# Kernel optimization log

Hardware: AMD Instinct MI355X
Metric: run time of the kernel (lower is better)

The kernel has to match this reference:

```python
import jax, jax.numpy as jnp
import numpy as np

EPS = 1e-12  # torch F.normalize eps


def _l2norm(x, axis):
    n = jnp.maximum(jnp.linalg.norm(x, axis=axis, keepdims=True), EPS)
    return x / n


def setup_inputs() -> dict:
    key = jax.random.key(0)
    k1, k2, k3, k4, k5 = jax.random.split(key, 5)
    N, E, IN_DIM, FAC_K, DIM_K = 100000, 1600000, 64, 4, 16
    all_emb = jax.random.normal(k1, (N, IN_DIM), dtype=jnp.float32) * 0.1
    W = jax.random.normal(k2, (FAC_K, IN_DIM, DIM_K), dtype=jnp.float32) * (1.0 / np.sqrt(IN_DIM))
    b = jax.random.normal(k3, (FAC_K, 1, DIM_K), dtype=jnp.float32) * 0.02
    row = jax.random.randint(k4, (E,), 0, N, dtype=jnp.int32)
    col = jax.random.randint(k5, (E,), 0, N, dtype=jnp.int32)
    return {"all_emb": all_emb, "W": W, "b": b, "row": row, "col": col, "iter_k": 2}


def reference(all_emb, W, b, row, col, iter_k):
    N = all_emb.shape[0]
    # factorized projection: [N, in_dim] x [K, in_dim, dk] -> [K, N, dk]
    fac = jnp.einsum('nd,kdf->knf', all_emb, W + b)
    fac = jax.nn.leaky_relu(fac, negative_slope=0.2)
    fac = _l2norm(fac, axis=2)

    new_fac = fac
    for _ in range(iter_k):
        head = new_fac[:, row]            # [K, E, dk]
        tail = fac[:, col]                # [K, E, dk]
        p_uv = jnp.sum(head * tail, axis=2)   # [K, E]
        p_uv = jax.nn.softmax(p_uv, axis=0)   # softmax over factors
        p_uv = jax.lax.stop_gradient(p_uv)    # original detaches attention
        msg = p_uv[:, :, None] * tail         # [K, E, dk]
        agg = jax.vmap(lambda m: jax.ops.segment_sum(m, row, num_segments=N))(msg)
        new_fac = _l2norm(fac + agg, axis=2)  # [K, N, dk]

    # torch.cat(list(new_fac_emb), dim=1) -> [N, K*dk]
    out = jnp.transpose(new_fac, (1, 0, 2)).reshape(N, -1)
    return out
```

## Files before the change

### kernel.cpp

```cpp
#include <hip/hip_runtime.h>

#define IN_DIM 64
#define FAC_K  4
#define DIM_K  16
#define SH     6
#define EPB    8192
#define CAP    3072

typedef _Float16 h2v __attribute__((ext_vector_type(2)));

__device__ inline int   h2i(h2v v) { return __builtin_bit_cast(int, v); }
__device__ inline h2v   i2h(int v) { return __builtin_bit_cast(h2v, v); }
__device__ inline h2v   pkh(float a, float b) {
    return __builtin_bit_cast(h2v, __builtin_amdgcn_cvt_pkrtz(a, b));
}

#if __has_builtin(__builtin_amdgcn_fdot2)
__device__ inline float FDOT2(h2v a, h2v b, float c) {
    return __builtin_amdgcn_fdot2(a, b, c, false);
}
#else
__device__ inline float FDOT2(h2v a, h2v b, float c) {
    return c + (float)a.x * (float)b.x + (float)a.y * (float)b.y;
}
#endif

__global__ __launch_bounds__(256) void fac_hist_kernel(
    const float* __restrict__ emb, const float* __restrict__ W,
    const float* __restrict__ b,   _Float16* __restrict__ fac16,
    const int* __restrict__ row,   int* __restrict__ H,
    int N, int E, int FB, int NB_blk, int NBUK)
{
    const int tid = threadIdx.x;

    if (blockIdx.x >= FB) {
        __shared__ int hist[2048];
        const int hb   = blockIdx.x - FB;
        const int base = hb * EPB;
        for (int i = tid; i < NBUK; i += 256) hist[i] = 0;
        __syncthreads();
#pragma unroll
        for (int i = 0; i < EPB / 256; ++i) {
            int e = base + i * 256 + tid;
            if (e < E) atomicAdd(&hist[row[e] >> SH], 1);
        }
        __syncthreads();
        for (int i = tid; i < NBUK; i += 256)
            H[(size_t)i * NB_blk + hb] = hist[i];
        return;
    }

    const int lane = tid & 63;
    const int wid  = (blockIdx.x * 256 + tid) >> 6;
    const int nwaves = FB * 4;
    const int k = lane >> 4, f = lane & 15;

    h2v wb2[32];
    const float bv = b[lane];
#pragma unroll
    for (int d = 0; d < 32; ++d) {
        float w0 = W[k * 1024 + (2 * d)     * 16 + f] + bv;
        float w1 = W[k * 1024 + (2 * d + 1) * 16 + f] + bv;
        wb2[d] = pkh(w0, w1);
    }

    for (int n = wid; n < N; n += nwaves) {
        const float4* er = (const float4*)(emb + (size_t)n * 64);
        float acc = 0.f;
#pragma unroll
        for (int j = 0; j < 16; ++j) {
            float4 e4 = er[j];
            acc = FDOT2(pkh(e4.x, e4.y), wb2[2 * j],     acc);
            acc = FDOT2(pkh(e4.z, e4.w), wb2[2 * j + 1], acc);
        }
        float v = acc > 0.f ? acc : 0.2f * acc;
        float s = v * v;
        s += __shfl_xor(s, 1);
        s += __shfl_xor(s, 2);
        s += __shfl_xor(s, 4);
        s += __shfl_xor(s, 8);
        v *= 1.0f / fmaxf(sqrtf(s), 1e-12f);
        fac16[(size_t)n * 64 + lane] = (_Float16)v;
    }
}

__global__ __launch_bounds__(1024) void scan1_kernel(
    const int* __restrict__ in, int* __restrict__ out,
    int* __restrict__ bsum, int M)
{
    __shared__ int wsum[16];
    const int tid  = threadIdx.x;
    const int lane = tid & 63;
    const int w    = tid >> 6;
    const int gi   = blockIdx.x * 1024 + tid;

    int sc = (gi < M) ? in[gi] : 0;
#pragma unroll
    for (int d = 1; d < 64; d <<= 1) {
        int y = __shfl_up(sc, d);
        if (lane >= d) sc += y;
    }
    if (lane == 63) wsum[w] = sc;
    __syncthreads();
    if (w == 0) {
        int v = (lane < 16) ? wsum[lane] : 0;
#pragma unroll
        for (int d = 1; d < 16; d <<= 1) {
            int y = __shfl_up(v, d);
            if (lane >= d) v += y;
        }
        if (lane < 16) wsum[lane] = v;
    }
    __syncthreads();
    if (w > 0) sc += wsum[w - 1];
    if (gi < M) out[gi + 1] = sc;
    if (tid == 1023) bsum[blockIdx.x] = sc;
    if (blockIdx.x == 0 && tid == 0) out[0] = 0;
}

__global__ __launch_bounds__(1024) void scan2_kernel(int* __restrict__ bsum, int nb)
{
    __shared__ int sm[1024];
    const int tid = threadIdx.x;
    sm[tid] = (tid < nb) ? bsum[tid] : 0;
    __syncthreads();
    for (int d = 1; d < 1024; d <<= 1) {
        int t = (tid >= d) ? sm[tid - d] : 0;
        __syncthreads();
        sm[tid] += t;
        __syncthreads();
    }
    if (tid < nb) bsum[tid] = (tid > 0) ? sm[tid - 1] : 0;
}

__global__ __launch_bounds__(256) void scatter1_kernel(
    const int* __restrict__ row, const int* __restrict__ col,
    const int* __restrict__ Hscan, const int* __restrict__ bsum,
    int* __restrict__ tmp, int E, int NB_blk, int NBUK)
{
    __shared__ int cur[2048];
    const int tid = threadIdx.x;
    const int jb  = blockIdx.x;
    const int base = jb * EPB;
    for (int i = tid; i < NBUK; i += 256) {
        int g = i * NB_blk + jb;
        int v = Hscan[g];
        if (g >= 1) v += bsum[(g - 1) >> 10];
        cur[i] = v;
    }
    __syncthreads();
#pragma unroll
    for (int it = 0; it < EPB / 256; ++it) {
        int e = base + it * 256 + tid;
        if (e < E) {
            int r = row[e];
            int pos = atomicAdd(&cur[r >> SH], 1);
            tmp[pos] = ((r & 63) << 17) | col[e];
        }
    }
}

__global__ __launch_bounds__(256, 4) void agg_kernel(
    const _Float16* __restrict__ fac16, const int* __restrict__ tmp,
    const int* __restrict__ Hscan, const int* __restrict__ bsum,
    float* __restrict__ nf_out, int E, int NB_blk, int NBUK, int N)
{
    __shared__ int csr[CAP];
    __shared__ int hist[64];
    __shared__ int curx[64];
    __shared__ int offl[65];

    const int tid = threadIdx.x;
    const int b   = blockIdx.x;

    const int g0 = b * NB_blk;
    const int gE = g0 + NB_blk;
    const int start = Hscan[g0] + (g0 >= 1 ? bsum[(g0 - 1) >> 10] : 0);
    const int end   = Hscan[gE] + bsum[(gE - 1) >> 10];
    const int cnt   = end - start;
    const bool fits = (cnt <= CAP);

    if (tid < 64) hist[tid] = 0;
    __syncthreads();
    if (fits) {
        for (int i = tid; i < cnt; i += 256)
            atomicAdd(&hist[tmp[start + i] >> 17], 1);
        __syncthreads();
        if (tid < 64) {
            int e = hist[tid];
            int sc = e;
#pragma unroll
            for (int d = 1; d < 64; d <<= 1) {
                int y = __shfl_up(sc, d);
                if (tid >= d) sc += y;
            }
            int ex = sc - e;
            offl[tid] = ex;
            curx[tid] = ex;
            if (tid == 63) offl[64] = sc;
        }
        __syncthreads();
        for (int i = tid; i < cnt; i += 256) {
            int u = tmp[start + i];
            int pos = atomicAdd(&curx[u >> 17], 1);
            csr[pos] = u & 0x1FFFF;
        }
    }
    __syncthreads();

    const int grp = tid >> 4;
    const int k   = tid & 3;
    const int q   = (tid >> 2) & 3;

    for (int round = 0; round < 4; ++round) {
        const int lr = round * 16 + grp;
        const int n  = (b << SH) + lr;
        if (n >= N) continue;

        const _Float16* frow = fac16 + (size_t)n * 64 + k * 16;
        uint4 fa = ((const uint4*)frow)[0];
        uint4 fb = ((const uint4*)frow)[1];
        h2v fh[8] = { i2h(fa.x), i2h(fa.y), i2h(fa.z), i2h(fa.w),
                      i2h(fb.x), i2h(fb.y), i2h(fb.z), i2h(fb.w) };
        float f32[16];
#pragma unroll
        for (int r = 0; r < 8; ++r) { f32[2*r] = (float)fh[r].x; f32[2*r+1] = (float)fh[r].y; }
        h2v hh[8];
#pragma unroll
        for (int r = 0; r < 8; ++r) hh[r] = fh[r];

        int s_l = 0, len = 0;
        if (fits) { s_l = offl[lr]; len = offl[lr + 1] - s_l; }

        float vv[16];
#pragma unroll 1
        for (int pass = 0; pass < 2; ++pass) {
            h2v acc2[8];
#pragma unroll
            for (int r = 0; r < 8; ++r) acc2[r] = h2v{(_Float16)0.f, (_Float16)0.f};

            if (fits) {
                if (len > 0) {
                    int e = (q < len) ? q : len - 1;
                    int cc = csr[s_l + e];
                    const uint4* tp = (const uint4*)(fac16 + (size_t)cc * 64 + k * 16);
                    uint4 ta = tp[0], tb = tp[1];
                    for (int i = 0; i < len; i += 4) {
                        uint4 a = ta, bb2 = tb;
                        const bool valid = (i + q) < len;
                        if (i + 4 < len) {
                            int e2 = i + 4 + q;
                            int c2 = csr[s_l + (e2 < len ? e2 : len - 1)];
                            const uint4* tp2 = (const uint4*)(fac16 + (size_t)c2 * 64 + k * 16);
                            ta = tp2[0]; tb = tp2[1];
                        }
                        h2v t2[8] = { i2h(a.x), i2h(a.y), i2h(a.z), i2h(a.w),
                                      i2h(bb2.x), i2h(bb2.y), i2h(bb2.z), i2h(bb2.w) };
                        float p = 0.f;
#pragma unroll
                        for (int r = 0; r < 8; ++r) p = FDOT2(hh[r], t2[r], p);
                        float exv = valid ? __expf(p) : 0.f;
                        float qs = exv + __shfl_xor(exv, 1);
                        qs += __shfl_xor(qs, 2);
                        float w = valid ? exv * __builtin_amdgcn_rcpf(qs) : 0.f;
                        _Float16 wh = (_Float16)w;
                        h2v w2; w2.x = wh; w2.y = wh;
#pragma unroll
                        for (int r = 0; r < 8; ++r) acc2[r] += w2 * t2[r];
                    }
                }
            } else {
                for (int i = 0; i < cnt; ++i) {
                    int u = tmp[start + i];
                    if ((u >> 17) != lr) continue;
                    int cc = u & 0x1FFFF;
                    const uint4* tp = (const uint4*)(fac16 + (size_t)cc * 64 + k * 16);
                    uint4 a = tp[0], bb2 = tp[1];
                    h2v t2[8] = { i2h(a.x), i2h(a.y), i2h(a.z), i2h(a.w),
                                  i2h(bb2.x), i2h(bb2.y), i2h(bb2.z), i2h(bb2.w) };
                    float p = 0.f;
#pragma unroll
                    for (int r = 0; r < 8; ++r) p = FDOT2(hh[r], t2[r], p);
                    float exv = __expf(p);
                    float qs = exv + __shfl_xor(exv, 1);
                    qs += __shfl_xor(qs, 2);
                    float w = (q == 0) ? exv * __builtin_amdgcn_rcpf(qs) : 0.f;
                    _Float16 wh = (_Float16)w;
                    h2v w2; w2.x = wh; w2.y = wh;
#pragma unroll
                    for (int r = 0; r < 8; ++r) acc2[r] += w2 * t2[r];
                }
            }

#pragma unroll
            for (int r = 0; r < 8; ++r) {
                acc2[r] += i2h(__shfl_xor(h2i(acc2[r]), 4));
                acc2[r] += i2h(__shfl_xor(h2i(acc2[r]), 8));
            }
            float ss = 0.f;
#pragma unroll
            for (int r = 0; r < 8; ++r) {
                vv[2*r]   = f32[2*r]   + (float)acc2[r].x;
                vv[2*r+1] = f32[2*r+1] + (float)acc2[r].y;
            }
#pragma unroll
            for (int d = 0; d < 16; ++d) ss = fmaf(vv[d], vv[d], ss);
            float inv = 1.0f / fmaxf(sqrtf(ss), 1e-12f);
#pragma unroll
            for (int d = 0; d < 16; ++d) vv[d] *= inv;
            if (pass == 0) {
#pragma unroll
                for (int r = 0; r < 8; ++r) {
                    h2v t; t.x = (_Float16)vv[2*r]; t.y = (_Float16)vv[2*r+1];
                    hh[r] = t;
                }
            }
        }

        float4 o;
        o.x = (q==0) ? vv[0]  : (q==1) ? vv[4]  : (q==2) ? vv[8]  : vv[12];
        o.y = (q==0) ? vv[1]  : (q==1) ? vv[5]  : (q==2) ? vv[9]  : vv[13];
        o.z = (q==0) ? vv[2]  : (q==1) ? vv[6]  : (q==2) ? vv[10] : vv[14];
        o.w = (q==0) ? vv[3]  : (q==1) ? vv[7]  : (q==2) ? vv[11] : vv[15];
        ((float4*)(nf_out + (size_t)n * 64 + k * 16))[q] = o;
    }
}

extern "C" void kernel_launch(void* const* d_in, const int* in_sizes, int n_in,
                              void* d_out, int out_size, void* d_ws, size_t ws_size,
                              hipStream_t stream) {
    const float* emb = (const float*)d_in[0];
    const float* W   = (const float*)d_in[1];
    const float* b   = (const float*)d_in[2];
    const int*   row = (const int*)d_in[3];
    const int*   col = (const int*)d_in[4];

    const int N = in_sizes[0] / IN_DIM;
    const int E = in_sizes[3];

    const int NBUK   = (N + 63) >> SH;
    const int NB_blk = (E + EPB - 1) / EPB;
    const int M      = NBUK * NB_blk;

    float* nf = (float*)d_out;

    _Float16* fac16 = (_Float16*)d_ws;
    int*      tmp   = (int*)(fac16 + (size_t)N * 64);
    int*      H     = tmp + E;
    int*      Hscan = H + M;
    int*      bsum  = Hscan + (M + 1);

    const int nb1 = (M + 1023) / 1024;
    const int FB  = 1024;

    fac_hist_kernel<<<FB + NB_blk, 256, 0, stream>>>(
        emb, W, b, fac16, row, H, N, E, FB, NB_blk, NBUK);
    scan1_kernel<<<nb1, 1024, 0, stream>>>(H, Hscan, bsum, M);
    scan2_kernel<<<1, 1024, 0, stream>>>(bsum, nb1);
    scatter1_kernel<<<NB_blk, 256, 0, stream>>>(row, col, Hscan, bsum, tmp, E, NB_blk, NBUK);
    agg_kernel<<<NBUK, 256, 0, stream>>>(fac16, tmp, Hscan, bsum, nf, E, NB_blk, NBUK, N);
}
```

Measured before the change: 235.5 us.

## Use MFMA for factor projection, deepen agg prefetch, raise occupancy

The per-node FDOT2 projection is replaced by 16x16x32 f16 MFMA tiles over 16 nodes, with an LDS transpose for the per-factor L2 normalisation and vectorised fp16 stores. The agg kernel's gather prefetch goes from one to two iterations ahead, its occupancy hint doubles by lowering the LDS CSR capacity from 3072 to 2048, and the projection grid is halved. A lower CAP sends more buckets down the slow non-fitting path, and the extra prefetch registers may spill under the tighter register budget.

```diff
diff --git a/kernel.cpp b/kernel.cpp
--- a/kernel.cpp
+++ b/kernel.cpp
@@ -5,9 +5,11 @@
 #define DIM_K  16
 #define SH     6
 #define EPB    8192
-#define CAP    3072
+#define CAP    2048
 
 typedef _Float16 h2v __attribute__((ext_vector_type(2)));
+typedef _Float16 h8v __attribute__((ext_vector_type(8)));
+typedef float    f4v __attribute__((ext_vector_type(4)));
 
 __device__ inline int   h2i(h2v v) { return __builtin_bit_cast(int, v); }
 __device__ inline h2v   i2h(int v) { return __builtin_bit_cast(h2v, v); }
@@ -24,6 +26,10 @@
     return c + (float)a.x * (float)b.x + (float)a.y * (float)b.y;
 }
 #endif
+
+union H8U { h8v v; h2v p[4]; };
+
+#define TSZ 1344
 
 __global__ __launch_bounds__(256) void fac_hist_kernel(
     const float* __restrict__ emb, const float* __restrict__ W,
@@ -31,10 +37,11 @@
     const int* __restrict__ row,   int* __restrict__ H,
     int N, int E, int FB, int NB_blk, int NBUK)
 {
+    __shared__ float lds_pool[4 * TSZ];
     const int tid = threadIdx.x;
 
     if (blockIdx.x >= FB) {
-        __shared__ int hist[2048];
+        int* hist = (int*)lds_pool;
         const int hb   = blockIdx.x - FB;
         const int base = hb * EPB;
         for (int i = tid; i < NBUK; i += 256) hist[i] = 0;
@@ -51,36 +58,80 @@
     }
 
     const int lane = tid & 63;
-    const int wid  = (blockIdx.x * 256 + tid) >> 6;
-    const int nwaves = FB * 4;
-    const int k = lane >> 4, f = lane & 15;
-
-    h2v wb2[32];
-    const float bv = b[lane];
-#pragma unroll
-    for (int d = 0; d < 32; ++d) {
-        float w0 = W[k * 1024 + (2 * d)     * 16 + f] + bv;
-        float w1 = W[k * 1024 + (2 * d + 1) * 16 + f] + bv;
-        wb2[d] = pkh(w0, w1);
-    }
-
-    for (int n = wid; n < N; n += nwaves) {
-        const float4* er = (const float4*)(emb + (size_t)n * 64);
-        float acc = 0.f;
-#pragma unroll
-        for (int j = 0; j < 16; ++j) {
-            float4 e4 = er[j];
-            acc = FDOT2(pkh(e4.x, e4.y), wb2[2 * j],     acc);
-            acc = FDOT2(pkh(e4.z, e4.w), wb2[2 * j + 1], acc);
-        }
-        float v = acc > 0.f ? acc : 0.2f * acc;
-        float s = v * v;
-        s += __shfl_xor(s, 1);
-        s += __shfl_xor(s, 2);
-        s += __shfl_xor(s, 4);
-        s += __shfl_xor(s, 8);
-        v *= 1.0f / fmaxf(sqrtf(s), 1e-12f);
-        fac16[(size_t)n * 64 + lane] = (_Float16)v;
+    const int l    = lane & 15;
+    const int q    = lane >> 4;
+    float* T = lds_pool + (tid >> 6) * TSZ;
+
+    H8U Bf[4][2];
+#pragma unroll
+    for (int t = 0; t < 4; ++t) {
+        const float bv = b[16 * t + l];
+#pragma unroll
+        for (int s = 0; s < 2; ++s) {
+            const float* wp = W + t * 1024 + (32 * s + 8 * q) * 16 + l;
+#pragma unroll
+            for (int jp = 0; jp < 4; ++jp) {
+                float w0 = wp[(2 * jp)     * 16] + bv;
+                float w1 = wp[(2 * jp + 1) * 16] + bv;
+                Bf[t][s].p[jp] = pkh(w0, w1);
+            }
+        }
+    }
+
+    const int ntiles = (N + 15) >> 4;
+    const int nw     = FB * 4;
+    const int wid    = (blockIdx.x * 256 + tid) >> 6;
+
+    for (int tile = wid; tile < ntiles; tile += nw) {
+        const int n0 = tile << 4;
+        int nm = n0 + l; if (nm >= N) nm = N - 1;
+
+        f4v acc[4];
+#pragma unroll
+        for (int t = 0; t < 4; ++t) acc[t] = f4v{0.f, 0.f, 0.f, 0.f};
+
+#pragma unroll
+        for (int s = 0; s < 2; ++s) {
+            const float4* ap = (const float4*)(emb + (size_t)nm * 64 + 32 * s + 8 * q);
+            float4 a0 = ap[0], a1 = ap[1];
+            H8U A;
+            A.p[0] = pkh(a0.x, a0.y); A.p[1] = pkh(a0.z, a0.w);
+            A.p[2] = pkh(a1.x, a1.y); A.p[3] = pkh(a1.z, a1.w);
+#pragma unroll
+            for (int t = 0; t < 4; ++t)
+                acc[t] = __builtin_amdgcn_mfma_f32_16x16x32_f16(A.v, Bf[t][s].v, acc[t], 0, 0, 0);
+        }
+
+#pragma unroll
+        for (int t = 0; t < 4; ++t) {
+            f4v v = acc[t];
+            f4v vr;
+#pragma unroll
+            for (int r = 0; r < 4; ++r)
+                vr[r] = fmaxf(v[r], 0.f) + 0.2f * fminf(v[r], 0.f);
+            const int o = 16 * t + l;
+            ((f4v*)(T + 20 * o + 16 * t + 4 * q))[0] = vr;
+        }
+        float vv[16];
+        float ss = 0.f;
+#pragma unroll
+        for (int i = 0; i < 16; ++i) {
+            float x = T[20 * (16 * q + i) + 16 * q + l];
+            vv[i] = x;
+            ss = fmaf(x, x, ss);
+        }
+        float inv = 1.0f / fmaxf(sqrtf(ss), 1e-12f);
+        H8U o0, o1;
+#pragma unroll
+        for (int jp = 0; jp < 4; ++jp) {
+            o0.p[jp] = pkh(vv[2 * jp]     * inv, vv[2 * jp + 1] * inv);
+            o1.p[jp] = pkh(vv[8 + 2 * jp] * inv, vv[9 + 2 * jp] * inv);
+        }
+        if (n0 + l < N) {
+            uint4* dst = (uint4*)(fac16 + (size_t)(n0 + l) * 64 + q * 16);
+            dst[0] = __builtin_bit_cast(uint4, o0.v);
+            dst[1] = __builtin_bit_cast(uint4, o1.v);
+        }
     }
 }
 
@@ -160,7 +211,7 @@
     }
 }
 
-__global__ __launch_bounds__(256, 4) void agg_kernel(
+__global__ __launch_bounds__(256, 8) void agg_kernel(
     const _Float16* __restrict__ fac16, const int* __restrict__ tmp,
     const int* __restrict__ Hscan, const int* __restrict__ bsum,
     float* __restrict__ nf_out, int E, int NB_blk, int NBUK, int N)
@@ -241,18 +292,23 @@
 
             if (fits) {
                 if (len > 0) {
-                    int e = (q < len) ? q : len - 1;
-                    int cc = csr[s_l + e];
-                    const uint4* tp = (const uint4*)(fac16 + (size_t)cc * 64 + k * 16);
-                    uint4 ta = tp[0], tb = tp[1];
+                    int e0 = (q < len) ? q : len - 1;
+                    const uint4* tp0 = (const uint4*)(fac16 + (size_t)csr[s_l + e0] * 64 + k * 16);
+                    uint4 ta0 = tp0[0], tb0 = tp0[1];
+                    uint4 ta1 = ta0, tb1 = tb0;
+                    if (len > 4) {
+                        int e1 = (4 + q < len) ? 4 + q : len - 1;
+                        const uint4* tp1 = (const uint4*)(fac16 + (size_t)csr[s_l + e1] * 64 + k * 16);
+                        ta1 = tp1[0]; tb1 = tp1[1];
+                    }
                     for (int i = 0; i < len; i += 4) {
-                        uint4 a = ta, bb2 = tb;
+                        uint4 a = ta0, bb2 = tb0;
+                        ta0 = ta1; tb0 = tb1;
                         const bool valid = (i + q) < len;
-                        if (i + 4 < len) {
-                            int e2 = i + 4 + q;
-                            int c2 = csr[s_l + (e2 < len ? e2 : len - 1)];
-                            const uint4* tp2 = (const uint4*)(fac16 + (size_t)c2 * 64 + k * 16);
-                            ta = tp2[0]; tb = tp2[1];
+                        if (i + 8 < len) {
+                            int e2 = (i + 8 + q < len) ? i + 8 + q : len - 1;
+                            const uint4* tp2 = (const uint4*)(fac16 + (size_t)csr[s_l + e2] * 64 + k * 16);
+                            ta1 = tp2[0]; tb1 = tp2[1];
                         }
                         h2v t2[8] = { i2h(a.x), i2h(a.y), i2h(a.z), i2h(a.w),
                                       i2h(bb2.x), i2h(bb2.y), i2h(bb2.z), i2h(bb2.w) };
@@ -351,7 +407,7 @@
     int*      bsum  = Hscan + (M + 1);
 
     const int nb1 = (M + 1023) / 1024;
-    const int FB  = 1024;
+    const int FB  = 512;
 
     fac_hist_kernel<<<FB + NB_blk, 256, 0, stream>>>(
         emb, W, b, fac16, row, H, N, E, FB, NB_blk, NBUK);
```

After: 223.0 us. 5.3% less time.
